# Performance work log

Measured on AMD Instinct MI355X. Metric: run time of the kernel, lower is better.

The kernel has to match this reference:

```python
import jax, jax.numpy as jnp
import numpy as np

NHID = 1024
HEADS = 16
SEQ = 2048
BATCH = 4


def gelu_bert(x):
    # paper variant: x * sigmoid(1.702 * x)
    return x * jax.nn.sigmoid(1.702 * x)


def setup_inputs() -> dict:
    key = jax.random.key(0)
    ks = jax.random.split(key, 20)
    s = 0.02
    inp = {
        "query": jax.random.normal(ks[0], (SEQ, BATCH, NHID), jnp.float32),
        "key": jax.random.normal(ks[1], (SEQ, BATCH, NHID), jnp.float32),
        "value": jax.random.normal(ks[2], (SEQ, BATCH, NHID), jnp.float32),
        # gating params (torch init is zeros/ones; randomize mildly for a nontrivial baseline)
        "qs_p": jax.random.normal(ks[3], (1, 1, NHID), jnp.float32) * s,
        "ks_p": jax.random.normal(ks[4], (1, 1, NHID), jnp.float32) * s,
        "vs_p": jax.random.normal(ks[5], (1, 1, NHID), jnp.float32) * s,
        # Overparam (vq): Linear(nhid, 2*nhid)
        "vq_w": jax.random.normal(ks[6], (2 * NHID, NHID), jnp.float32) * s,
        "vq_b": jax.random.normal(ks[7], (2 * NHID,), jnp.float32) * s,
        # q/k/v projections: Linear(nhid, nhid)
        "q_w": jax.random.normal(ks[8], (NHID, NHID), jnp.float32) * s,
        "q_b": jax.random.normal(ks[9], (NHID,), jnp.float32) * s,
        "k_w": jax.random.normal(ks[10], (NHID, NHID), jnp.float32) * s,
        "k_b": jax.random.normal(ks[11], (NHID,), jnp.float32) * s,
        "v_w": jax.random.normal(ks[12], (NHID, NHID), jnp.float32) * s,
        "v_b": jax.random.normal(ks[13], (NHID,), jnp.float32) * s,
        # residual gate: Linear(2*nhid, nhid)
        "r_w": jax.random.normal(ks[14], (NHID, 2 * NHID), jnp.float32) * s,
        "r_b": jax.random.normal(ks[15], (NHID,), jnp.float32) * s,
        "r_gate": jnp.ones((1, 1, NHID), jnp.float32),
    }
    return inp


def reference(query, key, value, qs_p, ks_p, vs_p, vq_w, vq_b,
              q_w, q_b, k_w, k_b, v_w, v_b, r_w, r_b, r_gate):
    dim = NHID // HEADS
    # sigmoid gates
    qs = jax.nn.sigmoid(qs_p)
    ksg = jax.nn.sigmoid(ks_p)
    vs0 = jax.nn.sigmoid(vs_p)
    # Overparam on vs: l1 -> split -> sigmoid(f) * tanh(c)
    cf = vs0 @ vq_w.T + vq_b           # [1,1,2*nhid]
    c, f = cf[..., :NHID], cf[..., NHID:]
    vs = jax.nn.sigmoid(f) * jnp.tanh(c)
    # linear projections
    query = query @ q_w.T + q_b
    key = key @ k_w.T + k_b
    value = value @ v_w.T + v_b
    # gated scaling
    q = qs * query                      # [S,B,nhid]
    k = ksg * key
    v = vs * value
    original_q = q
    # to batch-first, then split heads -> [B,H,S,d]
    def split_heads(x):
        x = jnp.transpose(x, (1, 0, 2))                 # [B,S,nhid]
        x = x.reshape(BATCH, -1, HEADS, dim)
        return jnp.transpose(x, (0, 2, 1, 3))           # [B,H,S,d]
    qh, kh, vh = split_heads(q), split_heads(k), split_heads(v)
    scores = jnp.einsum('bhqd,bhkd->bhqk', qh, kh) / jnp.sqrt(jnp.float32(dim))
    weights = jax.nn.softmax(scores, axis=-1)           # [B,H,Sq,Sk]
    mix = jnp.einsum('bhqk,bhkd->bhqd', weights, vh)    # [B,H,S,d]
    mix = jnp.transpose(mix, (0, 2, 1, 3)).reshape(BATCH, -1, NHID)  # [B,S,nhid]
    mix = jnp.transpose(mix, (1, 0, 2))                 # [S,B,nhid]
    # residual gate MLP
    rcat = jnp.concatenate([mix, original_q], axis=-1)  # [S,B,2*nhid]
    r = gelu_bert(rcat @ r_w.T + r_b)
    out = jax.nn.sigmoid(r_gate) * mix + r
    return out
```

## Files before the change

### kernel.cpp

```cpp
#include <hip/hip_runtime.h>
#include <hip/hip_bf16.h>
#include <math.h>

#define SEQ   2048
#define BATCH 4
#define NHID  1024
#define HEADS 16
#define DIM   64
#define MROWS (SEQ*BATCH)
#define LOG2E 1.44269504f

typedef __attribute__((ext_vector_type(8)))  short bf16x8;
typedef __attribute__((ext_vector_type(4)))  float f32x4;
typedef __attribute__((ext_vector_type(16))) float f32x16;

__device__ __forceinline__ float sigf(float x) { return 1.0f / (1.0f + expf(-x)); }

__device__ __forceinline__ unsigned short f2b(float x) {
    unsigned int u = __float_as_uint(x);
    return (unsigned short)((u + 0x7FFFu + ((u >> 16) & 1u)) >> 16);
}
__device__ __forceinline__ float b2f(unsigned short h) {
    return __uint_as_float(((unsigned int)h) << 16);
}
__device__ __forceinline__ unsigned pk2(float lo, float hi) {
    __hip_bfloat162 h = __float22bfloat162_rn(make_float2(lo, hi));
    union { __hip_bfloat162 h; unsigned u; } cv; cv.h = h;
    return cv.u;
}
__device__ __forceinline__ float fexp2(float x) {
    float tf = __builtin_fmaf(x, 8388608.0f, 1065103216.0f);
    return __uint_as_float((unsigned)(int)tf);
}
__device__ __forceinline__ void gload_lds16(const void* g, void* l) {
    __builtin_amdgcn_global_load_lds((const __attribute__((address_space(1))) void*)g,
                                     (__attribute__((address_space(3))) void*)l,
                                     16, 0, 0);
}

__global__ __launch_bounds__(256) void k_f2b_all(const float* __restrict__ s0,
                                                 const float* __restrict__ s1,
                                                 const float* __restrict__ s2,
                                                 const float* __restrict__ s3,
                                                 unsigned short* __restrict__ d0,
                                                 unsigned short* __restrict__ d1,
                                                 unsigned short* __restrict__ d2,
                                                 unsigned short* __restrict__ d3)
{
    int blk = blockIdx.x;
    const float* src; unsigned short* dst;
    if      (blk < 1024) { src = s0; dst = d0; }
    else if (blk < 2048) { src = s1; dst = d1; blk -= 1024; }
    else if (blk < 3072) { src = s2; dst = d2; blk -= 2048; }
    else                 { src = s3; dst = d3; blk -= 3072; }
    const int i = (blk * 256 + threadIdx.x) * 4;
    float4 v = *(const float4*)(src + i);
    unsigned long long pack = (unsigned long long)f2b(v.x)
                            | ((unsigned long long)f2b(v.y) << 16)
                            | ((unsigned long long)f2b(v.z) << 32)
                            | ((unsigned long long)f2b(v.w) << 48);
    *(unsigned long long*)(dst + i) = pack;
}

__global__ __launch_bounds__(256) void k_cf(const float* __restrict__ vs_p,
                                            const float* __restrict__ vq_w,
                                            const float* __restrict__ vq_b,
                                            float* __restrict__ cf)
{
    const int wave = threadIdx.x >> 6, lane = threadIdx.x & 63;
    const int j = blockIdx.x * 4 + wave;
    const float* w = vq_w + (size_t)j * NHID;
    float p = 0.f;
    for (int i = lane; i < NHID; i += 64) p += sigf(vs_p[i]) * w[i];
#pragma unroll
    for (int off = 32; off; off >>= 1) p += __shfl_down(p, off);
    if (lane == 0) cf[j] = p + vq_b[j];
}

__global__ __launch_bounds__(256) void k_scales(const float* __restrict__ qs_p,
                                                const float* __restrict__ ks_p,
                                                const float* __restrict__ r_gate,
                                                const float* __restrict__ cf,
                                                float* __restrict__ sq, float* __restrict__ sk,
                                                float* __restrict__ sv, float* __restrict__ rg)
{
    for (int n = threadIdx.x; n < NHID; n += 256) {
        sq[n] = sigf(qs_p[n]);
        sk[n] = sigf(ks_p[n]) * (0.125f * LOG2E);
        rg[n] = sigf(r_gate[n]);
        sv[n] = sigf(cf[n + NHID]) * tanhf(cf[n]);
    }
}

#define GEMM_FRAGS(K)                                                            \
        _Pragma("unroll")                                                        \
        for (int ks = 0; ks < 2; ++ks) {                                         \
            bf16x8 af[4], bf[4];                                                 \
            _Pragma("unroll")                                                    \
            for (int mi = 0; mi < 4; ++mi) {                                     \
                const int r  = wr * 64 + mi * 16 + (lane & 15);                  \
                const int c8 = (ks * 4 + (lane >> 4)) ^ (r & 7);                 \
                af[mi] = *(const bf16x8*)&As[r * 64 + c8 * 8];                   \
            }                                                                    \
            _Pragma("unroll")                                                    \
            for (int ni = 0; ni < 4; ++ni) {                                     \
                const int r  = wc * 64 + ni * 16 + (lane & 15);                  \
                const int c8 = (ks * 4 + (lane >> 4)) ^ (r & 7);                 \
                bf[ni] = *(const bf16x8*)&Bs[r * 64 + c8 * 8];                   \
            }                                                                    \
            _Pragma("unroll")                                                    \
            for (int mi = 0; mi < 4; ++mi)                                       \
                _Pragma("unroll")                                                \
                for (int ni = 0; ni < 4; ++ni)                                   \
                    acc[mi][ni] = __builtin_amdgcn_mfma_f32_16x16x32_bf16(af[mi], bf[ni], acc[mi][ni], 0, 0, 0); \
        }

__global__ __launch_bounds__(256) void k_proj3(const float* __restrict__ A0,
                                               const float* __restrict__ A1,
                                               const float* __restrict__ A2,
                                               const unsigned short* __restrict__ W0,
                                               const unsigned short* __restrict__ W1,
                                               const unsigned short* __restrict__ W2,
                                               const float* __restrict__ b0,
                                               const float* __restrict__ b1,
                                               const float* __restrict__ b2,
                                               const float* __restrict__ c0,
                                               const float* __restrict__ c1,
                                               const float* __restrict__ c2,
                                               unsigned short* __restrict__ o0,
                                               unsigned short* __restrict__ o1,
                                               unsigned short* __restrict__ o2)
{
    __shared__ unsigned short As[128 * 64];
    __shared__ unsigned short Bs[128 * 64];
    const int t = threadIdx.x;
    const int wid = t >> 6, lane = t & 63;
    const int wr = wid >> 1, wc = wid & 1;
    int f = blockIdx.x;
    int wg = (f & 7) * 192 + (f >> 3);
    const int seg = wg / 512, inner = wg - seg * 512;
    const int bm = inner >> 3, bn = inner & 7;
    const float* A = seg == 0 ? A0 : seg == 1 ? A1 : A2;
    const unsigned short* W = seg == 0 ? W0 : seg == 1 ? W1 : W2;
    const float* bias  = seg == 0 ? b0 : seg == 1 ? b1 : b2;
    const float* scale = seg == 0 ? c0 : seg == 1 ? c1 : c2;
    unsigned short* outb = seg == 0 ? o0 : seg == 1 ? o1 : o2;
    const float* Ab = A + (size_t)bm * 128 * NHID;
    const unsigned short* Bb = W + (size_t)bn * 128 * NHID;

    f32x4 acc[4][4] = {};

    for (int k0 = 0; k0 < NHID; k0 += 64) {
        __syncthreads();
#pragma unroll
        for (int it = 0; it < 4; ++it) {
            const int c    = it * 256 + t;
            const int row  = c >> 3;
            const int col8 = c & 7;
            const int g8   = col8 ^ (row & 7);
            gload_lds16(Bb + (size_t)row * NHID + k0 + g8 * 8, (char*)Bs + c * 16);
            const float* ap = Ab + (size_t)row * NHID + k0 + col8 * 8;
            float4 x0 = *(const float4*)ap;
            float4 x1 = *(const float4*)(ap + 4);
            union { unsigned w[4]; bf16x8 v; } pa;
            pa.w[0] = pk2(x0.x, x0.y); pa.w[1] = pk2(x0.z, x0.w);
            pa.w[2] = pk2(x1.x, x1.y); pa.w[3] = pk2(x1.z, x1.w);
            *(bf16x8*)&As[row * 64 + g8 * 8] = pa.v;
        }
        __syncthreads();
        GEMM_FRAGS(NHID)
    }

#pragma unroll
    for (int mi = 0; mi < 4; ++mi) {
#pragma unroll
        for (int r = 0; r < 4; ++r) {
            const int m = bm * 128 + wr * 64 + mi * 16 + (lane >> 4) * 4 + r;
#pragma unroll
            for (int ni = 0; ni < 4; ++ni) {
                const int n = bn * 128 + wc * 64 + ni * 16 + (lane & 15);
                const float v = scale[n] * (acc[mi][ni][r] + bias[n]);
                if (seg == 0) {
                    outb[(size_t)m * 2048 + 1024 + n] = f2b(v);
                } else {
                    const int s = m >> 2, b = m & 3, h = n >> 6, d = n & 63;
                    outb[((size_t)(b * HEADS + h) * SEQ + s) * DIM + d] = f2b(v);
                }
            }
        }
    }
}

__global__ __launch_bounds__(256) void k_final(const unsigned short* __restrict__ A,
                                               const unsigned short* __restrict__ W,
                                               const float* __restrict__ bias,
                                               const float* __restrict__ rg,
                                               float* __restrict__ outf,
                                               const unsigned short* __restrict__ mixb)
{
    __shared__ unsigned short As[128 * 64];
    __shared__ unsigned short Bs[128 * 64];
    const int t = threadIdx.x;
    const int wid = t >> 6, lane = t & 63;
    const int wr = wid >> 1, wc = wid & 1;
    int wg = blockIdx.y * 64 + blockIdx.x;
    wg = (wg & 7) * 64 + (wg >> 3);
    const int bm = wg >> 3, bn = wg & 7;
    const int K = 2 * NHID;
    const unsigned short* Ab = A + (size_t)bm * 128 * K;
    const unsigned short* Bb = W + (size_t)bn * 128 * K;

    f32x4 acc[4][4] = {};
    for (int k0 = 0; k0 < K; k0 += 64) {
        __syncthreads();
#pragma unroll
        for (int it = 0; it < 4; ++it) {
            const int c   = it * 256 + t;
            const int row = c >> 3;
            const int g8  = (c & 7) ^ (row & 7);
            gload_lds16(Ab + (size_t)row * K + k0 + g8 * 8, (char*)As + c * 16);
            gload_lds16(Bb + (size_t)row * K + k0 + g8 * 8, (char*)Bs + c * 16);
        }
        __syncthreads();
        GEMM_FRAGS(K)
    }

#pragma unroll
    for (int mi = 0; mi < 4; ++mi) {
#pragma unroll
        for (int r = 0; r < 4; ++r) {
            const int m = bm * 128 + wr * 64 + mi * 16 + (lane >> 4) * 4 + r;
#pragma unroll
            for (int ni = 0; ni < 4; ++ni) {
                const int n = bn * 128 + wc * 64 + ni * 16 + (lane & 15);
                const float pre = acc[mi][ni][r] + bias[n];
                const float g = pre * sigf(1.702f * pre);
                const float mx = b2f(mixb[(size_t)m * 2048 + n]);
                outf[(size_t)m * NHID + n] = rg[n] * mx + g;
            }
        }
    }
}

__global__ __launch_bounds__(256) void k_vt(const unsigned short* __restrict__ Vin,
                                            unsigned short* __restrict__ Vout)
{
    __shared__ unsigned short Ls[64][66];
    const int bh = blockIdx.x >> 5, st = blockIdx.x & 31;
    const int t = threadIdx.x;
    const unsigned short* src = Vin + ((size_t)bh * SEQ + st * 64) * DIM;
    {
        const int s = t >> 2, d0 = (t & 3) * 16;
        *(bf16x8*)&Ls[s][d0]     = *(const bf16x8*)&src[s * DIM + d0];
        *(bf16x8*)&Ls[s][d0 + 8] = *(const bf16x8*)&src[s * DIM + d0 + 8];
    }
    __syncthreads();
    const int d = t >> 2, s0 = (t & 3) * 16;
    union { unsigned short h[16]; unsigned long long q[4]; } r;
#pragma unroll
    for (int i = 0; i < 16; ++i) r.h[i] = Ls[s0 + i][d];
    unsigned short* dst = Vout + ((size_t)bh * DIM + d) * SEQ + st * 64 + s0;
    *(unsigned long long*)&dst[0]  = r.q[0];
    *(unsigned long long*)&dst[8]  = r.q[1];
    *(unsigned long long*)&dst[4]  = r.q[2];
    *(unsigned long long*)&dst[12] = r.q[3];
}

#define LDS8(BASE, ROW, C8) \
    (*(const bf16x8*)&(BASE)[((ROW) << 6) + ((((C8) ^ ((ROW) & 7))) << 3)])

#define STAGE(KB, VB, J0) do {                                                   \
    _Pragma("unroll")                                                            \
    for (int it_ = 0; it_ < 2; ++it_) {                                          \
        const int ch_  = it_ * 256 + t;                                          \
        const int row_ = ch_ >> 3;                                               \
        const int c8_  = (ch_ & 7) ^ (row_ & 7);                                 \
        gload_lds16(Kbh + (size_t)((J0) + row_) * DIM + c8_ * 8,                 \
                    (char*)(KB) + ch_ * 16);                                     \
        gload_lds16(Vbh + (size_t)row_ * SEQ + (J0) + c8_ * 8,                   \
                    (char*)(VB) + ch_ * 16);                                     \
    }                                                                            \
} while (0)

#define TILE(KB, VB) do {                                                        \
    f32x16 sA = {}, sB = {};                                                     \
    __builtin_amdgcn_s_setprio(1);                                               \
    _Pragma("unroll")                                                            \
    for (int ds_ = 0; ds_ < 4; ++ds_) {                                          \
        bf16x8 kf0 = LDS8(KB, q31,      ds_ * 2 + g2);                           \
        bf16x8 kf1 = LDS8(KB, 32 + q31, ds_ * 2 + g2);                           \
        sA = __builtin_amdgcn_mfma_f32_32x32x16_bf16(kf0, qf[ds_], sA, 0, 0, 0); \
        sB = __builtin_amdgcn_mfma_f32_32x32x16_bf16(kf1, qf[ds_], sB, 0, 0, 0); \
    }                                                                            \
    __builtin_amdgcn_s_setprio(0);                                               \
    unsigned ppk[16];                                                            \
    _Pragma("unroll")                                                            \
    for (int p = 0; p < 8; ++p) {                                                \
        ppk[p]     = pk2(fexp2(sA[2 * p]), fexp2(sA[2 * p + 1]));                \
        ppk[8 + p] = pk2(fexp2(sB[2 * p]), fexp2(sB[2 * p + 1]));                \
    }                                                                            \
    f32x16 accP = {};                                                            \
    __builtin_amdgcn_s_setprio(1);                                               \
    _Pragma("unroll")                                                            \
    for (int kc = 0; kc < 4; ++kc) {                                             \
        union { unsigned w[4]; bf16x8 v; } up;                                   \
        up.w[0] = ppk[4 * kc + 0];                                               \
        up.w[1] = ppk[4 * kc + 1];                                               \
        up.w[2] = ppk[4 * kc + 2];                                               \
        up.w[3] = ppk[4 * kc + 3];                                               \
        bf16x8 vf0 = LDS8(VB, q31,      kc * 2 + g2);                            \
        bf16x8 vf1 = LDS8(VB, 32 + q31, kc * 2 + g2);                            \
        accP  = __builtin_amdgcn_mfma_f32_32x32x16_bf16(aone.v, up.v, accP, 0, 0, 0);\
        accO0 = __builtin_amdgcn_mfma_f32_32x32x16_bf16(vf0, up.v, accO0, 0, 0, 0);\
        accO1 = __builtin_amdgcn_mfma_f32_32x32x16_bf16(vf1, up.v, accO1, 0, 0, 0);\
    }                                                                            \
    __builtin_amdgcn_s_setprio(0);                                               \
    l_r += accP[0];                                                              \
} while (0)

__global__ __launch_bounds__(256, 4) void k_attn(const unsigned short* __restrict__ Qc,
                                                 const unsigned short* __restrict__ Kb,
                                                 const unsigned short* __restrict__ Vt,
                                                 unsigned short* __restrict__ mixo)
{
    __shared__ unsigned short Ks0[4096], Ks1[4096];
    __shared__ unsigned short Vs0[4096], Vs1[4096];
    const int t = threadIdx.x, wid = t >> 6, l = t & 63;
    const int g2 = l >> 5, q31 = l & 31;
    const int f = blockIdx.x;
    const int bh = (f & 7) + ((f >> 7) << 3);
    const int qt = (f >> 3) & 15;
    const int b = bh >> 4, h = bh & 15;
    const int s_q = qt * 128 + wid * 32 + q31;

    const unsigned short* Kbh = Kb + (size_t)bh * SEQ * DIM;
    const unsigned short* Vbh = Vt + (size_t)bh * DIM * SEQ;
    const unsigned short* Qrow = Qc + (size_t)(s_q * 4 + b) * 2048 + 1024 + h * 64;

    bf16x8 qf[4];
#pragma unroll
    for (int ds_ = 0; ds_ < 4; ++ds_)
        qf[ds_] = *(const bf16x8*)&Qrow[ds_ * 16 + g2 * 8];

    union { unsigned w[4]; bf16x8 v; } aone;
    aone.w[0] = aone.w[1] = aone.w[2] = aone.w[3] = 0x3F803F80u;

    f32x16 accO0 = {}, accO1 = {};
    float l_r = 0.f;

    STAGE(Ks0, Vs0, 0);
#pragma unroll 1
    for (int j0 = 0; j0 < SEQ; j0 += 128) {
        __syncthreads();
        if (j0 + 64 < SEQ) STAGE(Ks1, Vs1, j0 + 64);
        TILE(Ks0, Vs0);
        __syncthreads();
        if (j0 + 128 < SEQ) STAGE(Ks0, Vs0, j0 + 128);
        TILE(Ks1, Vs1);
    }

    const float inv = 1.f / l_r;
    unsigned short* dst = mixo + (size_t)(s_q * 4 + b) * 2048 + h * 64;
#pragma unroll
    for (int reg = 0; reg < 16; reg += 2) {
        const int d0a = (reg & 3) + 8 * (reg >> 2) + 4 * g2;
        *(unsigned*)&dst[d0a]      = pk2(accO0[reg] * inv, accO0[reg + 1] * inv);
        *(unsigned*)&dst[32 + d0a] = pk2(accO1[reg] * inv, accO1[reg + 1] * inv);
    }
}

extern "C" void kernel_launch(void* const* d_in, const int* in_sizes, int n_in,
                              void* d_out, int out_size, void* d_ws, size_t ws_size,
                              hipStream_t stream)
{
    (void)in_sizes; (void)n_in; (void)out_size; (void)ws_size;
    const float* query  = (const float*)d_in[0];
    const float* key    = (const float*)d_in[1];
    const float* value  = (const float*)d_in[2];
    const float* qs_p   = (const float*)d_in[3];
    const float* ks_p   = (const float*)d_in[4];
    const float* vs_p   = (const float*)d_in[5];
    const float* vq_w   = (const float*)d_in[6];
    const float* vq_b   = (const float*)d_in[7];
    const float* q_w    = (const float*)d_in[8];
    const float* q_b    = (const float*)d_in[9];
    const float* k_w    = (const float*)d_in[10];
    const float* k_b    = (const float*)d_in[11];
    const float* v_w    = (const float*)d_in[12];
    const float* v_b    = (const float*)d_in[13];
    const float* r_w    = (const float*)d_in[14];
    const float* r_b    = (const float*)d_in[15];
    const float* r_gate = (const float*)d_in[16];

    float* fws = (float*)d_ws;
    float* sq = fws;
    float* sk = fws + 1024;
    float* sv = fws + 2048;
    float* rg = fws + 3072;
    float* cf = fws + 4096;

    unsigned short* uws = (unsigned short*)(fws + 8192);
    unsigned short* Wq = uws;
    unsigned short* Wk = Wq + (size_t)NHID * NHID;
    unsigned short* Wv = Wk + (size_t)NHID * NHID;
    unsigned short* Wr = Wv + (size_t)NHID * NHID;
    unsigned short* Qc = Wr + (size_t)NHID * 2 * NHID;
    unsigned short* Kb = Qc + (size_t)MROWS * 2 * NHID;
    unsigned short* Vb = Kb + (size_t)BATCH * HEADS * SEQ * DIM;
    unsigned short* Vtmp = Vb + (size_t)BATCH * HEADS * SEQ * DIM;

    k_cf<<<dim3(512), dim3(256), 0, stream>>>(vs_p, vq_w, vq_b, cf);
    k_scales<<<dim3(1), dim3(256), 0, stream>>>(qs_p, ks_p, r_gate, cf, sq, sk, sv, rg);

    k_f2b_all<<<dim3(5120), dim3(256), 0, stream>>>(q_w, k_w, v_w, r_w,
                                                    Wq, Wk, Wv, Wr);

    k_proj3<<<dim3(1536), dim3(256), 0, stream>>>(query, key, value, Wq, Wk, Wv,
                                                  q_b, k_b, v_b, sq, sk, sv,
                                                  Qc, Kb, Vtmp);
    k_vt<<<dim3(2048), dim3(256), 0, stream>>>(Vtmp, Vb);

    k_attn<<<dim3(1024), dim3(256), 0, stream>>>(Qc, Kb, Vb, Qc);

    k_final<<<dim3(64, 8), dim3(256), 0, stream>>>(Qc, Wr, r_b, rg, (float*)d_out, Qc);
}
```

Before: 272.9 us.

## Stream fp32 activations directly into LDS in projection GEMM and merge prep kernels

The projection GEMM now loads fp32 A tiles straight into LDS with async global_load_lds, and converts them to bf16 only when reading MFMA fragments, instead of loading through registers and converting before the LDS store. The K step shrinks from 64 to 32 so the fp32 tile fits in a similar LDS footprint, which doubles the number of barrier rounds. The cf dot-product kernel and the weight bf16 conversion kernel are merged into one launch to save a kernel launch. The trade-off is more loop iterations and syncs against less register staging and better load/compute overlap.

```diff
diff --git a/kernel.cpp b/kernel.cpp
--- a/kernel.cpp
+++ b/kernel.cpp
@@ -38,16 +38,31 @@
                                      16, 0, 0);
 }
 
-__global__ __launch_bounds__(256) void k_f2b_all(const float* __restrict__ s0,
-                                                 const float* __restrict__ s1,
-                                                 const float* __restrict__ s2,
-                                                 const float* __restrict__ s3,
-                                                 unsigned short* __restrict__ d0,
-                                                 unsigned short* __restrict__ d1,
-                                                 unsigned short* __restrict__ d2,
-                                                 unsigned short* __restrict__ d3)
-{
-    int blk = blockIdx.x;
+__global__ __launch_bounds__(256) void k_prep(const float* __restrict__ vs_p,
+                                              const float* __restrict__ vq_w,
+                                              const float* __restrict__ vq_b,
+                                              float* __restrict__ cf,
+                                              const float* __restrict__ s0,
+                                              const float* __restrict__ s1,
+                                              const float* __restrict__ s2,
+                                              const float* __restrict__ s3,
+                                              unsigned short* __restrict__ d0,
+                                              unsigned short* __restrict__ d1,
+                                              unsigned short* __restrict__ d2,
+                                              unsigned short* __restrict__ d3)
+{
+    if (blockIdx.x < 512) {
+        const int wave = threadIdx.x >> 6, lane = threadIdx.x & 63;
+        const int j = blockIdx.x * 4 + wave;
+        const float* w = vq_w + (size_t)j * NHID;
+        float p = 0.f;
+        for (int i = lane; i < NHID; i += 64) p += sigf(vs_p[i]) * w[i];
+#pragma unroll
+        for (int off = 32; off; off >>= 1) p += __shfl_down(p, off);
+        if (lane == 0) cf[j] = p + vq_b[j];
+        return;
+    }
+    int blk = blockIdx.x - 512;
     const float* src; unsigned short* dst;
     if      (blk < 1024) { src = s0; dst = d0; }
     else if (blk < 2048) { src = s1; dst = d1; blk -= 1024; }
@@ -62,21 +77,6 @@
     *(unsigned long long*)(dst + i) = pack;
 }
 
-__global__ __launch_bounds__(256) void k_cf(const float* __restrict__ vs_p,
-                                            const float* __restrict__ vq_w,
-                                            const float* __restrict__ vq_b,
-                                            float* __restrict__ cf)
-{
-    const int wave = threadIdx.x >> 6, lane = threadIdx.x & 63;
-    const int j = blockIdx.x * 4 + wave;
-    const float* w = vq_w + (size_t)j * NHID;
-    float p = 0.f;
-    for (int i = lane; i < NHID; i += 64) p += sigf(vs_p[i]) * w[i];
-#pragma unroll
-    for (int off = 32; off; off >>= 1) p += __shfl_down(p, off);
-    if (lane == 0) cf[j] = p + vq_b[j];
-}
-
 __global__ __launch_bounds__(256) void k_scales(const float* __restrict__ qs_p,
                                                 const float* __restrict__ ks_p,
                                                 const float* __restrict__ r_gate,
@@ -91,29 +91,6 @@
         sv[n] = sigf(cf[n + NHID]) * tanhf(cf[n]);
     }
 }
-
-#define GEMM_FRAGS(K)                                                            \
-        _Pragma("unroll")                                                        \
-        for (int ks = 0; ks < 2; ++ks) {                                         \
-            bf16x8 af[4], bf[4];                                                 \
-            _Pragma("unroll")                                                    \
-            for (int mi = 0; mi < 4; ++mi) {                                     \
-                const int r  = wr * 64 + mi * 16 + (lane & 15);                  \
-                const int c8 = (ks * 4 + (lane >> 4)) ^ (r & 7);                 \
-                af[mi] = *(const bf16x8*)&As[r * 64 + c8 * 8];                   \
-            }                                                                    \
-            _Pragma("unroll")                                                    \
-            for (int ni = 0; ni < 4; ++ni) {                                     \
-                const int r  = wc * 64 + ni * 16 + (lane & 15);                  \
-                const int c8 = (ks * 4 + (lane >> 4)) ^ (r & 7);                 \
-                bf[ni] = *(const bf16x8*)&Bs[r * 64 + c8 * 8];                   \
-            }                                                                    \
-            _Pragma("unroll")                                                    \
-            for (int mi = 0; mi < 4; ++mi)                                       \
-                _Pragma("unroll")                                                \
-                for (int ni = 0; ni < 4; ++ni)                                   \
-                    acc[mi][ni] = __builtin_amdgcn_mfma_f32_16x16x32_bf16(af[mi], bf[ni], acc[mi][ni], 0, 0, 0); \
-        }
 
 __global__ __launch_bounds__(256) void k_proj3(const float* __restrict__ A0,
                                                const float* __restrict__ A1,
@@ -131,8 +108,8 @@
                                                unsigned short* __restrict__ o1,
                                                unsigned short* __restrict__ o2)
 {
-    __shared__ unsigned short As[128 * 64];
-    __shared__ unsigned short Bs[128 * 64];
+    __shared__ float          Asf[128 * 32];
+    __shared__ unsigned short Bs[128 * 32];
     const int t = threadIdx.x;
     const int wid = t >> 6, lane = t & 63;
     const int wr = wid >> 1, wc = wid & 1;
@@ -150,25 +127,49 @@
 
     f32x4 acc[4][4] = {};
 
-    for (int k0 = 0; k0 < NHID; k0 += 64) {
+    for (int k0 = 0; k0 < NHID; k0 += 32) {
         __syncthreads();
 #pragma unroll
         for (int it = 0; it < 4; ++it) {
-            const int c    = it * 256 + t;
-            const int row  = c >> 3;
-            const int col8 = c & 7;
-            const int g8   = col8 ^ (row & 7);
-            gload_lds16(Bb + (size_t)row * NHID + k0 + g8 * 8, (char*)Bs + c * 16);
-            const float* ap = Ab + (size_t)row * NHID + k0 + col8 * 8;
-            float4 x0 = *(const float4*)ap;
-            float4 x1 = *(const float4*)(ap + 4);
+            const int c   = it * 256 + t;
+            const int row = c >> 3;
+            const int g   = (c & 7) ^ (row & 7);
+            gload_lds16(Ab + (size_t)row * NHID + k0 + g * 4, (char*)Asf + c * 16);
+        }
+#pragma unroll
+        for (int it = 0; it < 2; ++it) {
+            const int c   = it * 256 + t;
+            const int row = c >> 2;
+            const int g   = (c & 3) ^ (row & 3);
+            gload_lds16(Bb + (size_t)row * NHID + k0 + g * 8, (char*)Bs + c * 16);
+        }
+        __syncthreads();
+
+        bf16x8 af[4], bf[4];
+#pragma unroll
+        for (int mi = 0; mi < 4; ++mi) {
+            const int r   = wr * 64 + mi * 16 + (lane & 15);
+            const int gc0 = (lane >> 4) * 2;
+            const int cl0 = gc0 ^ (r & 7);
+            const int cl1 = (gc0 + 1) ^ (r & 7);
+            f32x4 v0 = *(const f32x4*)&Asf[r * 32 + cl0 * 4];
+            f32x4 v1 = *(const f32x4*)&Asf[r * 32 + cl1 * 4];
             union { unsigned w[4]; bf16x8 v; } pa;
-            pa.w[0] = pk2(x0.x, x0.y); pa.w[1] = pk2(x0.z, x0.w);
-            pa.w[2] = pk2(x1.x, x1.y); pa.w[3] = pk2(x1.z, x1.w);
-            *(bf16x8*)&As[row * 64 + g8 * 8] = pa.v;
-        }
-        __syncthreads();
-        GEMM_FRAGS(NHID)
+            pa.w[0] = pk2(v0[0], v0[1]); pa.w[1] = pk2(v0[2], v0[3]);
+            pa.w[2] = pk2(v1[0], v1[1]); pa.w[3] = pk2(v1[2], v1[3]);
+            af[mi] = pa.v;
+        }
+#pragma unroll
+        for (int ni = 0; ni < 4; ++ni) {
+            const int r  = wc * 64 + ni * 16 + (lane & 15);
+            const int cl = (lane >> 4) ^ (r & 3);
+            bf[ni] = *(const bf16x8*)&Bs[r * 32 + cl * 8];
+        }
+#pragma unroll
+        for (int mi = 0; mi < 4; ++mi)
+#pragma unroll
+            for (int ni = 0; ni < 4; ++ni)
+                acc[mi][ni] = __builtin_amdgcn_mfma_f32_16x16x32_bf16(af[mi], bf[ni], acc[mi][ni], 0, 0, 0);
     }
 
 #pragma unroll
@@ -222,7 +223,27 @@
             gload_lds16(Bb + (size_t)row * K + k0 + g8 * 8, (char*)Bs + c * 16);
         }
         __syncthreads();
-        GEMM_FRAGS(K)
+#pragma unroll
+        for (int ks = 0; ks < 2; ++ks) {
+            bf16x8 af[4], bf[4];
+#pragma unroll
+            for (int mi = 0; mi < 4; ++mi) {
+                const int r  = wr * 64 + mi * 16 + (lane & 15);
+                const int c8 = (ks * 4 + (lane >> 4)) ^ (r & 7);
+                af[mi] = *(const bf16x8*)&As[r * 64 + c8 * 8];
+            }
+#pragma unroll
+            for (int ni = 0; ni < 4; ++ni) {
+                const int r  = wc * 64 + ni * 16 + (lane & 15);
+                const int c8 = (ks * 4 + (lane >> 4)) ^ (r & 7);
+                bf[ni] = *(const bf16x8*)&Bs[r * 64 + c8 * 8];
+            }
+#pragma unroll
+            for (int mi = 0; mi < 4; ++mi)
+#pragma unroll
+                for (int ni = 0; ni < 4; ++ni)
+                    acc[mi][ni] = __builtin_amdgcn_mfma_f32_16x16x32_bf16(af[mi], bf[ni], acc[mi][ni], 0, 0, 0);
+        }
     }
 
 #pragma unroll
@@ -409,11 +430,10 @@
     unsigned short* Vb = Kb + (size_t)BATCH * HEADS * SEQ * DIM;
     unsigned short* Vtmp = Vb + (size_t)BATCH * HEADS * SEQ * DIM;
 
-    k_cf<<<dim3(512), dim3(256), 0, stream>>>(vs_p, vq_w, vq_b, cf);
+    k_prep<<<dim3(5632), dim3(256), 0, stream>>>(vs_p, vq_w, vq_b, cf,
+                                                 q_w, k_w, v_w, r_w,
+                                                 Wq, Wk, Wv, Wr);
     k_scales<<<dim3(1), dim3(256), 0, stream>>>(qs_p, ks_p, r_gate, cf, sq, sk, sv, rg);
-
-    k_f2b_all<<<dim3(5120), dim3(256), 0, stream>>>(q_w, k_w, v_w, r_w,
-                                                    Wq, Wk, Wv, Wr);
 
     k_proj3<<<dim3(1536), dim3(256), 0, stream>>>(query, key, value, Wq, Wk, Wv,
                                                   q_b, k_b, v_b, sq, sk, sv,
```

Result: faster. 257.3 us (-5.7%).
